# Performance work log

Hardware: AMD Instinct MI355X
Metric: run time of the kernel (lower is better)

## Reference

```python
import jax, jax.numpy as jnp
import numpy as np

N, C, H, W = 8, 64, 256, 256
HO, WO = 256, 256


def setup_inputs() -> dict:
    key = jax.random.key(0)
    kx, kg = jax.random.split(key)
    x = jax.random.normal(kx, (N, C, H, W), dtype=jnp.float32)
    # normalized sampling coords in [-1, 1], last dim = (x, y)
    grid = jax.random.uniform(kg, (N, HO, WO, 2), dtype=jnp.float32, minval=-1.0, maxval=1.0)
    return {"x": x, "grid": grid}


def reference(x, grid):
    # Bilinear grid sample, align_corners=True, border-clamped indices
    # x: [N, C, H, W]; grid: [N, Ho, Wo, 2] in [-1, 1]
    n, c, h, w = x.shape
    ix = (grid[..., 0] + 1.0) * 0.5 * (w - 1)  # [N, Ho, Wo] unnormalized x coord
    iy = (grid[..., 1] + 1.0) * 0.5 * (h - 1)

    x0f = jnp.floor(ix)
    y0f = jnp.floor(iy)
    wx1 = ix - x0f  # frac weights
    wy1 = iy - y0f
    wx0 = 1.0 - wx1
    wy0 = 1.0 - wy1

    x0 = jnp.clip(x0f, 0, w - 1).astype(jnp.int32)
    x1 = jnp.clip(x0f + 1.0, 0, w - 1).astype(jnp.int32)
    y0 = jnp.clip(y0f, 0, h - 1).astype(jnp.int32)
    y1 = jnp.clip(y0f + 1.0, 0, h - 1).astype(jnp.int32)

    xt = jnp.transpose(x, (0, 2, 3, 1))  # [N, H, W, C] for channels-last gather
    b = jnp.arange(n)[:, None, None]  # [N, 1, 1] batch index

    def gather(yi, xi):
        return xt[b, yi, xi]  # [N, Ho, Wo, C]

    out = (gather(y0, x0) * (wy0 * wx0)[..., None]
           + gather(y0, x1) * (wy0 * wx1)[..., None]
           + gather(y1, x0) * (wy1 * wx0)[..., None]
           + gather(y1, x1) * (wy1 * wx1)[..., None])
    return jnp.transpose(out, (0, 3, 1, 2))  # [N, C, Ho, Wo]
```

## Files before the change

kernel.cpp:

```cpp
#include <hip/hip_runtime.h>
#include <hip/hip_bf16.h>


constexpr int N = 8, C = 64, H = 256, W = 256, HO = 256, WO = 256;
constexpr int NPIX = N * HO * WO;
constexpr int PLANE = H * W;
constexpr size_t XT_BYTES = (size_t)N * PLANE * C * sizeof(unsigned short);

typedef unsigned short ushortv8 __attribute__((ext_vector_type(8)));
typedef float floatx4 __attribute__((ext_vector_type(4)));

__device__ __forceinline__ float bf16_to_f(unsigned short u) {
  union { unsigned int i; float f; } v;
  v.i = ((unsigned int)u) << 16;
  return v.f;
}

__global__ __launch_bounds__(256) void transpose_kernel(
    const float* __restrict__ x, unsigned int* __restrict__ xt) {
  __shared__ float tile[64][65];
  int tx = threadIdx.x;
  int ty = threadIdx.y;
  int t = (ty << 6) + tx;
  int tileIdx = blockIdx.x;
  int n = tileIdx >> 10;
  int pixb = (tileIdx & 1023) << 6;

  const float* xn = x + (size_t)n * C * PLANE;
#pragma unroll
  for (int k = 0; k < 16; ++k) {
    int c = (k << 2) + ty;
    tile[c][tx] = __builtin_nontemporal_load(&xn[(size_t)c * PLANE + pixb + tx]);
  }
  __syncthreads();

  unsigned int* xtw = xt + ((size_t)(n * PLANE + pixb)) * 32;
  int chp = t & 31;
#pragma unroll
  for (int k = 0; k < 8; ++k) {
    int p = (k << 3) + (t >> 5);
    float f0 = tile[2 * chp][p];
    float f1 = tile[2 * chp + 1][p];
    __hip_bfloat162 h2 = __float22bfloat162_rn(make_float2(f0, f1));
    unsigned int w;
    __builtin_memcpy(&w, &h2, 4);
    xtw[(size_t)p * 32 + chp] = w;
  }
}

__global__ __launch_bounds__(256, 4) void sample_kernel(
    const unsigned short* __restrict__ xt, const float* __restrict__ grid,
    float* __restrict__ out) {
  __shared__ float tile[4][64][33];

  int tid  = threadIdx.x;
  int wid  = tid >> 6;
  int lane = tid & 63;
  int pixb = (blockIdx.x << 8) + (wid << 6);
  int p_idx = pixb + lane;
  int n = p_idx >> 16;

  float2 g = ((const float2*)grid)[p_idx];
  float ix = (g.x + 1.0f) * 0.5f * (float)(W - 1);
  float iy = (g.y + 1.0f) * 0.5f * (float)(H - 1);
  float x0f = floorf(ix), y0f = floorf(iy);
  float fx = ix - x0f, fy = iy - y0f;
  float cx0 = fminf(fmaxf(x0f,        0.f), (float)(W - 1));
  float cx1 = fminf(fmaxf(x0f + 1.f,  0.f), (float)(W - 1));
  float cy0 = fminf(fmaxf(y0f,        0.f), (float)(H - 1));
  float cy1 = fminf(fmaxf(y0f + 1.f,  0.f), (float)(H - 1));
  int x0 = (int)cx0, x1 = (int)cx1, y0 = (int)cy0, y1 = (int)cy1;
  int xl = min(x0, W - 2), yl = min(y0, H - 2);
  float wx0 = 1.f - fx, wx1 = fx, wy0 = 1.f - fy, wy1 = fy;
  float wxl = (x0 == xl ? wx0 : 0.f) + (x1 == xl ? wx1 : 0.f);
  float wxh = (x0 == xl + 1 ? wx0 : 0.f) + (x1 == xl + 1 ? wx1 : 0.f);
  float wyl = (y0 == yl ? wy0 : 0.f) + (y1 == yl ? wy1 : 0.f);
  float wyh = (y0 == yl + 1 ? wy0 : 0.f) + (y1 == yl + 1 ? wy1 : 0.f);
  float w00 = wyl * wxl, w01 = wyl * wxh, w10 = wyh * wxl, w11 = wyh * wxh;
  int bs = ((n << 16) | (yl << 8) | xl) << 6;

  int ps    = lane >> 3;
  int chunk = lane & 7;
  const unsigned short* xtc = xt + (chunk << 3);
  float (*tl)[33] = tile[wid];

  int prow = pixb & (PLANE - 1);
  float* outn = out + (size_t)n * C * PLANE + prow;

  ushortv8 A[3][4];

#define ISSUE(gg, slot)                                                        \
  {                                                                            \
    int p = ((gg) << 3) + ps;                                                  \
    int bsp = __shfl(bs, p);                                                   \
    const ushortv8* src = (const ushortv8*)(xtc + bsp);                        \
    A[slot][0] = src[0];                                                       \
    A[slot][1] = src[C / 8];                                                   \
    A[slot][2] = src[(C * W) / 8];                                             \
    A[slot][3] = src[(C * W + C) / 8];                                         \
  }

  ISSUE(0, 0)
  ISSUE(1, 1)

#pragma unroll
  for (int gq = 0; gq < 8; ++gq) {
    if (gq + 2 < 8) {
      const int sl = (gq + 2) % 3;
      ISSUE(gq + 2, sl)
    }
    {
      const int sl = gq % 3;
      int p = (gq << 3) + ps;
      float wa = __shfl(w00, p), wb = __shfl(w01, p);
      float wc = __shfl(w10, p), wd = __shfl(w11, p);
      int ph = ((gq & 3) << 3) + ps;
#pragma unroll
      for (int jp = 0; jp < 4; ++jp) {
        unsigned int ua = ((unsigned int*)&A[sl][0])[jp];
        unsigned int ub = ((unsigned int*)&A[sl][1])[jp];
        unsigned int uc = ((unsigned int*)&A[sl][2])[jp];
        unsigned int ud = ((unsigned int*)&A[sl][3])[jp];
        float a0 = __uint_as_float(ua << 16), a1 = __uint_as_float(ua & 0xffff0000u);
        float b0 = __uint_as_float(ub << 16), b1 = __uint_as_float(ub & 0xffff0000u);
        float c0 = __uint_as_float(uc << 16), c1 = __uint_as_float(uc & 0xffff0000u);
        float d0 = __uint_as_float(ud << 16), d1 = __uint_as_float(ud & 0xffff0000u);
        float r0 = a0 * wa + b0 * wb + c0 * wc + d0 * wd;
        float r1 = a1 * wa + b1 * wb + c1 * wc + d1 * wd;
        int ch = (chunk << 3) + (jp << 1);
        tl[ch][ph]     = r0;
        tl[ch + 1][ph] = r1;
      }
    }
    if ((gq & 3) == 3) {
      int h = gq >> 2;
      int cs = lane >> 3;
      int q  = lane & 7;
#pragma unroll
      for (int k = 0; k < 8; ++k) {
        int c = (k << 3) + cs;
        floatx4 v = *(floatx4*)&tl[c][q << 2];
        __builtin_nontemporal_store(
            v, (floatx4*)(outn + (size_t)c * PLANE + (h << 5) + (q << 2)));
      }
    }
  }
#undef ISSUE
}

__global__ __launch_bounds__(256) void grid_sample_fallback(
    const float* __restrict__ x, const float* __restrict__ grid,
    float* __restrict__ out) {
  int idx = blockIdx.x * blockDim.x + threadIdx.x;
  if (idx >= NPIX) return;
  int wo = idx & (WO - 1);
  int ho = (idx >> 8) & (HO - 1);
  int n  = idx >> 16;
  float2 g = ((const float2*)grid)[idx];
  float ix = (g.x + 1.0f) * 0.5f * (float)(W - 1);
  float iy = (g.y + 1.0f) * 0.5f * (float)(H - 1);
  float x0f = floorf(ix), y0f = floorf(iy);
  float wx1 = ix - x0f, wy1 = iy - y0f;
  float wx0 = 1.0f - wx1, wy0 = 1.0f - wy1;
  int x0 = (int)fminf(fmaxf(x0f,        0.0f), (float)(W - 1));
  int x1 = (int)fminf(fmaxf(x0f + 1.0f, 0.0f), (float)(W - 1));
  int y0 = (int)fminf(fmaxf(y0f,        0.0f), (float)(H - 1));
  int y1 = (int)fminf(fmaxf(y0f + 1.0f, 0.0f), (float)(H - 1));
  float w00 = wy0 * wx0, w01 = wy0 * wx1, w10 = wy1 * wx0, w11 = wy1 * wx1;
  int o00 = y0 * W + x0, o01 = y0 * W + x1, o10 = y1 * W + x0, o11 = y1 * W + x1;
  const float* xn = x + (size_t)n * C * PLANE;
  float* on = out + (size_t)n * C * PLANE + (size_t)ho * WO + wo;
#pragma unroll 4
  for (int c = 0; c < C; ++c) {
    const float* xc = xn + c * PLANE;
    float v = xc[o00] * w00 + xc[o01] * w01 + xc[o10] * w10 + xc[o11] * w11;
    __builtin_nontemporal_store(v, on + (size_t)c * PLANE);
  }
}

extern "C" void kernel_launch(void* const* d_in, const int* in_sizes, int n_in,
                              void* d_out, int out_size, void* d_ws, size_t ws_size,
                              hipStream_t stream) {
  const float* x    = (const float*)d_in[0];
  const float* grid = (const float*)d_in[1];
  float* out        = (float*)d_out;

  if (ws_size >= XT_BYTES) {
    transpose_kernel<<<N * PLANE / 64, dim3(64, 4), 0, stream>>>(
        x, (unsigned int*)d_ws);
    sample_kernel<<<NPIX / 256, 256, 0, stream>>>(
        (const unsigned short*)d_ws, grid, out);
  } else {
    grid_sample_fallback<<<NPIX / 256, 256, 0, stream>>>(x, grid, out);
  }
}
```

Before: 263.5 us.

## Vectorize transpose loads/stores and interleave batches across blocks

The transpose kernel now loads four floats per thread with 16-byte nontemporal loads and writes 16-byte nontemporal packed bf16 stores, instead of scalar loads and 4-byte stores. It also switches to a 1D 256-thread block. Both kernels now map consecutive block indices to different batch images (n = b & 7), spreading concurrent blocks across batches, which may change cache and channel locality. The float4 LDS writes into the padded 65-wide tile may cause bank conflicts.

```diff
diff --git a/kernel.cpp b/kernel.cpp
--- a/kernel.cpp
+++ b/kernel.cpp
@@ -9,42 +9,45 @@
 
 typedef unsigned short ushortv8 __attribute__((ext_vector_type(8)));
 typedef float floatx4 __attribute__((ext_vector_type(4)));
-
-__device__ __forceinline__ float bf16_to_f(unsigned short u) {
-  union { unsigned int i; float f; } v;
-  v.i = ((unsigned int)u) << 16;
-  return v.f;
-}
+typedef unsigned int uintx4 __attribute__((ext_vector_type(4)));
 
 __global__ __launch_bounds__(256) void transpose_kernel(
     const float* __restrict__ x, unsigned int* __restrict__ xt) {
   __shared__ float tile[64][65];
-  int tx = threadIdx.x;
-  int ty = threadIdx.y;
-  int t = (ty << 6) + tx;
-  int tileIdx = blockIdx.x;
-  int n = tileIdx >> 10;
-  int pixb = (tileIdx & 1023) << 6;
-
-  const float* xn = x + (size_t)n * C * PLANE;
-#pragma unroll
-  for (int k = 0; k < 16; ++k) {
-    int c = (k << 2) + ty;
-    tile[c][tx] = __builtin_nontemporal_load(&xn[(size_t)c * PLANE + pixb + tx]);
+  int t = threadIdx.x;
+  int b = blockIdx.x;
+  int n = b & 7;
+  int pixb = (b >> 3) << 6;
+
+  const float* xn = x + (size_t)n * C * PLANE + pixb;
+  int px4 = (t & 15) << 2;
+  int c0  = t >> 4;
+#pragma unroll
+  for (int k = 0; k < 4; ++k) {
+    int c = c0 + (k << 4);
+    floatx4 v = __builtin_nontemporal_load(
+        (const floatx4*)(xn + (size_t)c * PLANE + px4));
+    *(floatx4*)&tile[c][px4] = v;
   }
   __syncthreads();
 
   unsigned int* xtw = xt + ((size_t)(n * PLANE + pixb)) * 32;
-  int chp = t & 31;
-#pragma unroll
-  for (int k = 0; k < 8; ++k) {
-    int p = (k << 3) + (t >> 5);
-    float f0 = tile[2 * chp][p];
-    float f1 = tile[2 * chp + 1][p];
-    __hip_bfloat162 h2 = __float22bfloat162_rn(make_float2(f0, f1));
-    unsigned int w;
-    __builtin_memcpy(&w, &h2, 4);
-    xtw[(size_t)p * 32 + chp] = w;
+  int chq = (t & 7) << 2;
+  int chb = chq << 1;
+#pragma unroll
+  for (int k = 0; k < 2; ++k) {
+    int p = (k << 5) + (t >> 3);
+    uintx4 wv;
+#pragma unroll
+    for (int j = 0; j < 4; ++j) {
+      float f0 = tile[chb + 2 * j][p];
+      float f1 = tile[chb + 2 * j + 1][p];
+      __hip_bfloat162 h2 = __float22bfloat162_rn(make_float2(f0, f1));
+      unsigned int w;
+      __builtin_memcpy(&w, &h2, 4);
+      wv[j] = w;
+    }
+    __builtin_nontemporal_store(wv, (uintx4*)(xtw + (size_t)p * 32 + chq));
   }
 }
 
@@ -56,9 +59,10 @@
   int tid  = threadIdx.x;
   int wid  = tid >> 6;
   int lane = tid & 63;
-  int pixb = (blockIdx.x << 8) + (wid << 6);
+  int b    = blockIdx.x;
+  int n    = b & 7;
+  int pixb = (n << 16) + ((b >> 3) << 8) + (wid << 6);
   int p_idx = pixb + lane;
-  int n = p_idx >> 16;
 
   float2 g = ((const float2*)grid)[p_idx];
   float ix = (g.x + 1.0f) * 0.5f * (float)(W - 1);
@@ -186,7 +190,7 @@
   float* out        = (float*)d_out;
 
   if (ws_size >= XT_BYTES) {
-    transpose_kernel<<<N * PLANE / 64, dim3(64, 4), 0, stream>>>(
+    transpose_kernel<<<N * PLANE / 64, 256, 0, stream>>>(
         x, (unsigned int*)d_ws);
     sample_kernel<<<NPIX / 256, 256, 0, stream>>>(
         (const unsigned short*)d_ws, grid, out);
```

New measurement: 281.2 us. 6.7% more time.
